# Kernel optimization log

Hardware: AMD Instinct MI355X
Metric: run time of the kernel (lower is better)

## Reference

```python
import jax, jax.numpy as jnp
import numpy as np

NUM_CODEBOOKS = 4
NUM_VECTORS = 1024
DIM = 256
B, T = 16, 4096


def setup_inputs() -> dict:
    key = jax.random.key(0)
    k1, k2 = jax.random.split(key)
    z = jax.random.normal(k1, (B, DIM, T), dtype=jnp.float32)
    # torch init: randn then uniform_(-1/num_vectors, 1/num_vectors) overwrites -> uniform
    codebooks = jax.random.uniform(
        k2, (NUM_CODEBOOKS, NUM_VECTORS, DIM), dtype=jnp.float32,
        minval=-1.0 / NUM_VECTORS, maxval=1.0 / NUM_VECTORS)
    return {"z": z, "codebooks": codebooks}


def reference(z, codebooks):
    # z: [B, C, T] -> work in token-major layout [B, T, C]
    x = jnp.transpose(z, (0, 2, 1))  # [B, T, C]
    sg = jax.lax.stop_gradient

    residual = x
    z_q = jnp.zeros_like(x)
    indices_list = []
    loss_total = jnp.float32(0.0)
    for i in range(codebooks.shape[0]):
        cb = codebooks[i]  # [V, C]
        # squared L2 distances: ||r||^2 + ||c||^2 - 2 r.c
        d = (jnp.sum(residual ** 2, axis=-1, keepdims=True)
             + jnp.sum(cb ** 2, axis=-1)
             - 2.0 * jnp.einsum('btc,vc->btv', residual, cb))  # [B, T, V]
        idx = jnp.argmin(d, axis=-1)        # [B, T]
        q = cb[idx]                          # [B, T, C] gather
        # straight-through estimator
        zq_i = residual + sg(q - residual)
        # commitment: mse(z_q.detach(), residual); z_q here equals q numerically
        loss_total = loss_total + jnp.mean((sg(zq_i) - residual) ** 2)
        z_q = z_q + zq_i
        residual = residual - sg(zq_i)
        indices_list.append(idx)

    loss = loss_total / codebooks.shape[0]
    indices = jnp.stack(indices_list, axis=1)      # [B, K, T]
    z_q_out = jnp.transpose(z_q, (0, 2, 1))        # [B, C, T]
    return z_q_out, indices, loss
```

## Files before the change

kernel.cpp:

```cpp
#include <hip/hip_runtime.h>
#include <math.h>

#define B_   16
#define C_   256
#define T_   4096
#define V_   1024
#define K_   4
#define TPB  64
#define EPS_CAND 2e-4f

constexpr int Z_ELEMS   = B_ * C_ * T_;
constexpr int IDX_ELEMS = B_ * K_ * T_;
constexpr int LOSS_OFF  = Z_ELEMS + IDX_ELEMS;

typedef _Float16 h8 __attribute__((ext_vector_type(8)));
typedef _Float16 h4 __attribute__((ext_vector_type(4)));
typedef float    f4 __attribute__((ext_vector_type(4)));

__global__ void rvq_zero_loss(float* out) { out[LOSS_OFF] = 0.0f; }

__global__ void rvq_cvnorm(const float* __restrict__ cb, float2* __restrict__ cvw)
{
    int g = blockIdx.x * 256 + threadIdx.x;
    const float* row = cb + (size_t)g * C_;
    float p0 = 0.f, p1 = 0.f;
    for (int c = 0;   c < 64;  ++c) p0 = fmaf(row[c], row[c], p0);
    for (int c = 128; c < 192; ++c) p0 = fmaf(row[c], row[c], p0);
    for (int c = 64;  c < 128; ++c) p1 = fmaf(row[c], row[c], p1);
    for (int c = 192; c < 256; ++c) p1 = fmaf(row[c], row[c], p1);
    cvw[g] = make_float2(p0, p1);
}

__global__ void rvq_cbf16(const float* __restrict__ cb, _Float16* __restrict__ cbh)
{
    int gid = blockIdx.x * 256 + threadIdx.x;
    int l  = gid & 63;
    int ks = (gid >> 6) & 7;
    int nt = (gid >> 9) & 63;
    int st = gid >> 15;
    int v  = nt * 16 + (l & 15);
    int k  = ks * 32 + (l >> 4) * 8;
    const float* src = cb + ((size_t)(st * V_ + v)) * C_ + k;
    float4 c0 = *reinterpret_cast<const float4*>(src);
    float4 c1 = *reinterpret_cast<const float4*>(src + 4);
    h8 o;
    o[0] = (_Float16)(c0.x * 16.0f);
    o[1] = (_Float16)(c0.y * 16.0f);
    o[2] = (_Float16)(c0.z * 16.0f);
    o[3] = (_Float16)(c0.w * 16.0f);
    o[4] = (_Float16)(c1.x * 16.0f);
    o[5] = (_Float16)(c1.y * 16.0f);
    o[6] = (_Float16)(c1.z * 16.0f);
    o[7] = (_Float16)(c1.w * 16.0f);
    reinterpret_cast<h8*>(cbh)[gid] = o;
}

__launch_bounds__(512, 1)
__global__ void rvq_main(const float* __restrict__ z,
                         const float* __restrict__ cb,
                         const float2* __restrict__ cvw,
                         const _Float16* __restrict__ cbh,
                         float* __restrict__ out)
{
    __shared__ float    Rt[C_][TPB];
    __shared__ _Float16 At[TPB * C_];
    __shared__ float    scratch[1024];
    __shared__ float    fminS[TPB];
    __shared__ int      candIdx[TPB][16];
    __shared__ int      candCnt[TPB];
    __shared__ int      bestIdx[TPB];
    __shared__ float    Rnorm[TPB];

    float* gminS  = scratch;
    float* pbD    = scratch;
    float* rnpart = reinterpret_cast<float*>(&candIdx[0][0]);
    char*  AtB    = reinterpret_cast<char*>(At);

    const int tid = threadIdx.x;
    const int blk = blockIdx.x;
    const int b   = blk >> 6;
    const int t0  = (blk & 63) * TPB;

    const int w   = tid >> 6;
    const int l   = tid & 63;
    const int ut  = tid & 63;
    const int ug  = tid >> 6;

    const int am   = l & 15;
    const int akof = (l >> 4) * 8;

    const float* zb = z + (size_t)b * C_ * T_ + t0;
    for (int j = 0; j < 32; ++j) {
        int c = ug * 32 + j;
        Rt[c][ut] = zb[(size_t)c * T_ + ut];
    }
    __syncthreads();
    {
        float p = 0.f;
        for (int j = 0; j < 32; ++j) { float r = Rt[ug * 32 + j][ut]; p = fmaf(r, r, p); }
        rnpart[ut * 8 + ug] = p;
    }
    #pragma unroll
    for (int j4 = 0; j4 < 8; ++j4) {
        int c0 = ug * 32 + 4 * j4;
        h4 hv;
        hv[0] = (_Float16)Rt[c0 + 0][ut];
        hv[1] = (_Float16)Rt[c0 + 1][ut];
        hv[2] = (_Float16)Rt[c0 + 2][ut];
        hv[3] = (_Float16)Rt[c0 + 3][ut];
        int off = (ut * 512 + c0 * 2) ^ ((ut & 7) << 4);
        *reinterpret_cast<h4*>(AtB + off) = hv;
    }
    __syncthreads();
    if (tid < TPB) {
        float s = rnpart[tid * 8];
        for (int k = 1; k < 8; ++k) s = __fadd_rn(s, rnpart[tid * 8 + k]);
        Rnorm[tid] = s;
    }
    __syncthreads();

    float loss_acc = 0.f;

    for (int st = 0; st < K_; ++st) {
        const float* cbs = cb + (size_t)st * V_ * C_;

        for (int p = 0; p < 2; ++p) {
            const int vbase = p * 512 + w * 64;

            f4 acc[4][4];
            #pragma unroll
            for (int mt = 0; mt < 4; ++mt)
                #pragma unroll
                for (int nf = 0; nf < 4; ++nf)
                    acc[mt][nf] = (f4){0.f, 0.f, 0.f, 0.f};

            {
                const h8* cbh8 = reinterpret_cast<const h8*>(cbh);
                const size_t wbase = (size_t)(st * 64 + (vbase >> 4)) * 512 + l;
                #pragma unroll 2
                for (int ks = 0; ks < 8; ++ks) {
                    h8 af[4];
                    #pragma unroll
                    for (int mt = 0; mt < 4; ++mt) {
                        int m = mt * 16 + am;
                        int off = (m * 512 + (ks * 32 + akof) * 2) ^ ((m & 7) << 4);
                        af[mt] = *reinterpret_cast<const h8*>(AtB + off);
                    }
                    #pragma unroll
                    for (int nf = 0; nf < 4; ++nf) {
                        h8 bf = cbh8[wbase + (size_t)nf * 512 + ks * 64];
                        #pragma unroll
                        for (int mt = 0; mt < 4; ++mt)
                            acc[mt][nf] = __builtin_amdgcn_mfma_f32_16x16x32_f16(af[mt], bf, acc[mt][nf], 0, 0, 0);
                    }
                }
            }

            #pragma unroll
            for (int nf = 0; nf < 4; ++nf) {
                int v = vbase + nf * 16 + am;
                float2 pv = cvw[st * V_ + v];
                float cv2 = __fadd_rn(pv.x, pv.y);
                #pragma unroll
                for (int mt = 0; mt < 4; ++mt)
                    #pragma unroll
                    for (int jj = 0; jj < 4; ++jj)
                        acc[mt][nf][jj] = fmaf(acc[mt][nf][jj], -0.125f, cv2);
            }

            #pragma unroll
            for (int mt = 0; mt < 4; ++mt)
                #pragma unroll
                for (int jj = 0; jj < 4; ++jj) {
                    float m0 = acc[mt][0][jj];
                    #pragma unroll
                    for (int nf = 1; nf < 4; ++nf) m0 = fminf(m0, acc[mt][nf][jj]);
                    m0 = fminf(m0, __shfl_xor(m0, 1, 16));
                    m0 = fminf(m0, __shfl_xor(m0, 2, 16));
                    m0 = fminf(m0, __shfl_xor(m0, 4, 16));
                    m0 = fminf(m0, __shfl_xor(m0, 8, 16));
                    if (am == 0)
                        gminS[w * 64 + mt * 16 + 4 * (l >> 4) + jj] = m0;
                }
            __syncthreads();

            if (tid < TPB) {
                float mm = gminS[tid];
                #pragma unroll
                for (int ww = 1; ww < 8; ++ww) mm = fminf(mm, gminS[ww * 64 + tid]);
                fminS[tid] = mm;
                if (p == 0) candCnt[tid] = 0;
            }
            __syncthreads();

            #pragma unroll
            for (int mt = 0; mt < 4; ++mt)
                #pragma unroll
                for (int jj = 0; jj < 4; ++jj) {
                    int t = mt * 16 + 4 * (l >> 4) + jj;
                    float fthr = fminS[t] + EPS_CAND;
                    #pragma unroll
                    for (int nf = 0; nf < 4; ++nf)
                        if (acc[mt][nf][jj] <= fthr) {
                            int s = atomicAdd(&candCnt[t], 1);
                            if (s < 16) candIdx[t][s] = vbase + nf * 16 + am;
                        }
                }
            __syncthreads();
        }

        {
            int t = tid & 63, s0 = tid >> 6;
            int nc = candCnt[t]; if (nc > 16) nc = 16;
            for (int s = s0; s < nc; s += 8) {
                int gi = candIdx[t][s];
                const float* crow = cbs + (size_t)gi * C_;
                float dot = 0.f;
                for (int c = 0; c < 256; c += 4) {
                    float4 cr = *reinterpret_cast<const float4*>(crow + c);
                    dot = __fadd_rn(dot, __fmul_rn(Rt[c + 0][t], cr.x));
                    dot = __fadd_rn(dot, __fmul_rn(Rt[c + 1][t], cr.y));
                    dot = __fadd_rn(dot, __fmul_rn(Rt[c + 2][t], cr.z));
                    dot = __fadd_rn(dot, __fmul_rn(Rt[c + 3][t], cr.w));
                }
                float2 pv = cvw[st * V_ + gi];
                float cv2 = __fadd_rn(pv.x, pv.y);
                float S = __fadd_rn(Rnorm[t], cv2);
                pbD[t * 16 + s] = __fsub_rn(S, 2.0f * dot);
            }
        }
        __syncthreads();
        if (tid < TPB) {
            int nc = candCnt[tid]; if (nc > 16) nc = 16;
            float bd = pbD[tid * 16];
            int   bi = candIdx[tid][0];
            for (int s = 1; s < nc; ++s) {
                float d  = pbD[tid * 16 + s];
                int   i2 = candIdx[tid][s];
                if (d < bd || (d == bd && i2 < bi)) { bd = d; bi = i2; }
            }
            bestIdx[tid] = bi;
            out[Z_ELEMS + ((size_t)b * K_ + st) * T_ + t0 + tid] = (float)bi;
        }
        __syncthreads();

        {
            const float* q = cbs + (size_t)bestIdx[ut] * C_ + ug * 32;
            float rn = 0.f;
            #pragma unroll
            for (int j4 = 0; j4 < 8; ++j4) {
                float4 qv = *reinterpret_cast<const float4*>(q + 4 * j4);
                float qe[4] = { qv.x, qv.y, qv.z, qv.w };
                h4 hv;
                #pragma unroll
                for (int e = 0; e < 4; ++e) {
                    int c = ug * 32 + 4 * j4 + e;
                    float r   = Rt[c][ut];
                    float qmr = __fsub_rn(qe[e], r);
                    float zq  = __fadd_rn(r, qmr);
                    float lt  = __fsub_rn(zq, r);
                    loss_acc  = fmaf(lt, lt, loss_acc);
                    float rn2 = __fsub_rn(r, zq);
                    Rt[c][ut] = rn2;
                    rn = fmaf(rn2, rn2, rn);
                    hv[e] = (_Float16)rn2;
                }
                int off = (ut * 512 + (ug * 32 + 4 * j4) * 2) ^ ((ut & 7) << 4);
                *reinterpret_cast<h4*>(AtB + off) = hv;
            }
            rnpart[ut * 8 + ug] = rn;
        }
        __syncthreads();
        if (tid < TPB) {
            float s = rnpart[tid * 8];
            for (int k = 1; k < 8; ++k) s = __fadd_rn(s, rnpart[tid * 8 + k]);
            Rnorm[tid] = s;
        }
        __syncthreads();
    }

    {
        float* ob = out + (size_t)b * C_ * T_ + t0;
        for (int j = 0; j < 32; ++j) {
            int c = ug * 32 + j;
            ob[(size_t)c * T_ + ut] = __fsub_rn(zb[(size_t)c * T_ + ut], Rt[c][ut]);
        }
    }

    __syncthreads();
    scratch[tid] = loss_acc;
    __syncthreads();
    if (tid < 256) scratch[tid] += scratch[tid + 256];
    __syncthreads();
    if (tid < 128) scratch[tid] += scratch[tid + 128];
    __syncthreads();
    if (tid < 64)  scratch[tid] += scratch[tid + 64];
    __syncthreads();
    if (tid == 0) {
        float s = 0.f;
        for (int i = 0; i < 64; ++i) s += scratch[i];
        atomicAdd(out + LOSS_OFF, s * (1.0f / 67108864.0f));
    }
}

extern "C" void kernel_launch(void* const* d_in, const int* in_sizes, int n_in,
                              void* d_out, int out_size, void* d_ws, size_t ws_size,
                              hipStream_t stream)
{
    const float* z  = (const float*)d_in[0];
    const float* cb = (const float*)d_in[1];
    float* out = (float*)d_out;
    float2*    cvw = (float2*)d_ws;
    _Float16*  cbh = (_Float16*)((char*)d_ws + 32768);

    rvq_zero_loss<<<1, 1, 0, stream>>>(out);
    rvq_cvnorm<<<16, 256, 0, stream>>>(cb, cvw);
    rvq_cbf16<<<512, 256, 0, stream>>>(cb, cbh);
    rvq_main<<<dim3(1024), dim3(512), 0, stream>>>(z, cb, cvw, cbh, out);
}
```

Baseline: 500.2 us.

## Drop fp16 residual copy, store residual token-major padded, convert on load

Replaces the channel-major fp32 residual plus separate swizzled fp16 copy with a single token-major padded fp32 array. The MFMA A-fragments are now converted from fp32 to fp16 on each load, the fp16 rewrite after each stage is removed, and the Rnorm reduction with its extra barrier is folded into the first pass of the next stage. Shared memory drops from about 100KB to about 75KB, and launch bounds are raised to 4 blocks per CU, aiming for two resident blocks per CU and fewer syncs. In exchange, every MFMA k-step does twice the LDS traffic plus conversion instructions, and the padded layout may cause bank conflicts.

```diff
diff --git a/kernel.cpp b/kernel.cpp
--- a/kernel.cpp
+++ b/kernel.cpp
@@ -7,6 +7,7 @@
 #define V_   1024
 #define K_   4
 #define TPB  64
+#define RFP  260
 #define EPS_CAND 2e-4f
 
 constexpr int Z_ELEMS   = B_ * C_ * T_;
@@ -14,7 +15,6 @@
 constexpr int LOSS_OFF  = Z_ELEMS + IDX_ELEMS;
 
 typedef _Float16 h8 __attribute__((ext_vector_type(8)));
-typedef _Float16 h4 __attribute__((ext_vector_type(4)));
 typedef float    f4 __attribute__((ext_vector_type(4)));
 
 __global__ void rvq_zero_loss(float* out) { out[LOSS_OFF] = 0.0f; }
@@ -55,26 +55,24 @@
     reinterpret_cast<h8*>(cbh)[gid] = o;
 }
 
-__launch_bounds__(512, 1)
+__launch_bounds__(512, 4)
 __global__ void rvq_main(const float* __restrict__ z,
                          const float* __restrict__ cb,
                          const float2* __restrict__ cvw,
                          const _Float16* __restrict__ cbh,
                          float* __restrict__ out)
 {
-    __shared__ float    Rt[C_][TPB];
-    __shared__ _Float16 At[TPB * C_];
-    __shared__ float    scratch[1024];
-    __shared__ float    fminS[TPB];
-    __shared__ int      candIdx[TPB][16];
-    __shared__ int      candCnt[TPB];
-    __shared__ int      bestIdx[TPB];
-    __shared__ float    Rnorm[TPB];
+    __shared__ float Rf[TPB][RFP];
+    __shared__ float scratch[1024];
+    __shared__ float fminS[TPB];
+    __shared__ int   candIdx[TPB][16];
+    __shared__ int   candCnt[TPB];
+    __shared__ int   bestIdx[TPB];
+    __shared__ float Rnorm[TPB];
 
     float* gminS  = scratch;
     float* pbD    = scratch;
     float* rnpart = reinterpret_cast<float*>(&candIdx[0][0]);
-    char*  AtB    = reinterpret_cast<char*>(At);
 
     const int tid = threadIdx.x;
     const int blk = blockIdx.x;
@@ -92,30 +90,20 @@
     const float* zb = z + (size_t)b * C_ * T_ + t0;
     for (int j = 0; j < 32; ++j) {
         int c = ug * 32 + j;
-        Rt[c][ut] = zb[(size_t)c * T_ + ut];
+        Rf[ut][c] = zb[(size_t)c * T_ + ut];
     }
     __syncthreads();
     {
         float p = 0.f;
-        for (int j = 0; j < 32; ++j) { float r = Rt[ug * 32 + j][ut]; p = fmaf(r, r, p); }
+        for (int j = 0; j < 32; ++j) { float r = Rf[ut][ug * 32 + j]; p = fmaf(r, r, p); }
         rnpart[ut * 8 + ug] = p;
-    }
-    #pragma unroll
-    for (int j4 = 0; j4 < 8; ++j4) {
-        int c0 = ug * 32 + 4 * j4;
-        h4 hv;
-        hv[0] = (_Float16)Rt[c0 + 0][ut];
-        hv[1] = (_Float16)Rt[c0 + 1][ut];
-        hv[2] = (_Float16)Rt[c0 + 2][ut];
-        hv[3] = (_Float16)Rt[c0 + 3][ut];
-        int off = (ut * 512 + c0 * 2) ^ ((ut & 7) << 4);
-        *reinterpret_cast<h4*>(AtB + off) = hv;
     }
     __syncthreads();
     if (tid < TPB) {
         float s = rnpart[tid * 8];
         for (int k = 1; k < 8; ++k) s = __fadd_rn(s, rnpart[tid * 8 + k]);
         Rnorm[tid] = s;
+        candCnt[tid] = 0;
     }
     __syncthreads();
 
@@ -139,12 +127,19 @@
                 const size_t wbase = (size_t)(st * 64 + (vbase >> 4)) * 512 + l;
                 #pragma unroll 2
                 for (int ks = 0; ks < 8; ++ks) {
+                    const int k0 = ks * 32 + akof;
                     h8 af[4];
                     #pragma unroll
                     for (int mt = 0; mt < 4; ++mt) {
-                        int m = mt * 16 + am;
-                        int off = (m * 512 + (ks * 32 + akof) * 2) ^ ((m & 7) << 4);
-                        af[mt] = *reinterpret_cast<const h8*>(AtB + off);
+                        const int m = mt * 16 + am;
+                        f4 x = *reinterpret_cast<const f4*>(&Rf[m][k0]);
+                        f4 y = *reinterpret_cast<const f4*>(&Rf[m][k0 + 4]);
+                        h8 a;
+                        a[0] = (_Float16)x[0]; a[1] = (_Float16)x[1];
+                        a[2] = (_Float16)x[2]; a[3] = (_Float16)x[3];
+                        a[4] = (_Float16)y[0]; a[5] = (_Float16)y[1];
+                        a[6] = (_Float16)y[2]; a[7] = (_Float16)y[3];
+                        af[mt] = a;
                     }
                     #pragma unroll
                     for (int nf = 0; nf < 4; ++nf) {
@@ -189,7 +184,11 @@
                 #pragma unroll
                 for (int ww = 1; ww < 8; ++ww) mm = fminf(mm, gminS[ww * 64 + tid]);
                 fminS[tid] = mm;
-                if (p == 0) candCnt[tid] = 0;
+                if (p == 0) {
+                    float s = rnpart[tid * 8];
+                    for (int k = 1; k < 8; ++k) s = __fadd_rn(s, rnpart[tid * 8 + k]);
+                    Rnorm[tid] = s;
+                }
             }
             __syncthreads();
 
@@ -218,10 +217,11 @@
                 float dot = 0.f;
                 for (int c = 0; c < 256; c += 4) {
                     float4 cr = *reinterpret_cast<const float4*>(crow + c);
-                    dot = __fadd_rn(dot, __fmul_rn(Rt[c + 0][t], cr.x));
-                    dot = __fadd_rn(dot, __fmul_rn(Rt[c + 1][t], cr.y));
-                    dot = __fadd_rn(dot, __fmul_rn(Rt[c + 2][t], cr.z));
-                    dot = __fadd_rn(dot, __fmul_rn(Rt[c + 3][t], cr.w));
+                    f4 rv = *reinterpret_cast<const f4*>(&Rf[t][c]);
+                    dot = __fadd_rn(dot, __fmul_rn(rv[0], cr.x));
+                    dot = __fadd_rn(dot, __fmul_rn(rv[1], cr.y));
+                    dot = __fadd_rn(dot, __fmul_rn(rv[2], cr.z));
+                    dot = __fadd_rn(dot, __fmul_rn(rv[3], cr.w));
                 }
                 float2 pv = cvw[st * V_ + gi];
                 float cv2 = __fadd_rn(pv.x, pv.y);
@@ -240,6 +240,7 @@
                 if (d < bd || (d == bd && i2 < bi)) { bd = d; bi = i2; }
             }
             bestIdx[tid] = bi;
+            candCnt[tid] = 0;
             out[Z_ELEMS + ((size_t)b * K_ + st) * T_ + t0 + tid] = (float)bi;
         }
         __syncthreads();
@@ -249,32 +250,25 @@
             float rn = 0.f;
             #pragma unroll
             for (int j4 = 0; j4 < 8; ++j4) {
+                int c0 = ug * 32 + 4 * j4;
                 float4 qv = *reinterpret_cast<const float4*>(q + 4 * j4);
+                f4 rv = *reinterpret_cast<const f4*>(&Rf[ut][c0]);
                 float qe[4] = { qv.x, qv.y, qv.z, qv.w };
-                h4 hv;
+                f4 nv;
                 #pragma unroll
                 for (int e = 0; e < 4; ++e) {
-                    int c = ug * 32 + 4 * j4 + e;
-                    float r   = Rt[c][ut];
+                    float r   = rv[e];
                     float qmr = __fsub_rn(qe[e], r);
                     float zq  = __fadd_rn(r, qmr);
                     float lt  = __fsub_rn(zq, r);
                     loss_acc  = fmaf(lt, lt, loss_acc);
                     float rn2 = __fsub_rn(r, zq);
-                    Rt[c][ut] = rn2;
+                    nv[e] = rn2;
                     rn = fmaf(rn2, rn2, rn);
-                    hv[e] = (_Float16)rn2;
-                }
-                int off = (ut * 512 + (ug * 32 + 4 * j4) * 2) ^ ((ut & 7) << 4);
-                *reinterpret_cast<h4*>(AtB + off) = hv;
+                }
+                *reinterpret_cast<f4*>(&Rf[ut][c0]) = nv;
             }
             rnpart[ut * 8 + ug] = rn;
-        }
-        __syncthreads();
-        if (tid < TPB) {
-            float s = rnpart[tid * 8];
-            for (int k = 1; k < 8; ++k) s = __fadd_rn(s, rnpart[tid * 8 + k]);
-            Rnorm[tid] = s;
         }
         __syncthreads();
     }
@@ -283,7 +277,7 @@
         float* ob = out + (size_t)b * C_ * T_ + t0;
         for (int j = 0; j < 32; ++j) {
             int c = ug * 32 + j;
-            ob[(size_t)c * T_ + ut] = __fsub_rn(zb[(size_t)c * T_ + ut], Rt[c][ut]);
+            ob[(size_t)c * T_ + ut] = __fsub_rn(zb[(size_t)c * T_ + ut], Rf[ut][c]);
         }
     }
 
```

Result: faster. 412.8 us (-17.5%).
